# Kernel tuning notes

Hardware: AMD Instinct MI355X
Metric: run time of the kernel (lower is better)

## Reference

```python
import jax, jax.numpy as jnp
import numpy as np

ANCHOR_SIZES = (128.0, 256.0, 512.0)
ASPECT_RATIOS = (0.5, 1.0, 2.0)
NMS_THR = 0.7
KEEP_PRE = 1000    # test_keep_pre_nms
KEEP_POST = 300    # test_keep_post_nms


def make_anchors(fh, fw, img_h, img_w):
    # base anchors per (ratio, size), centered at origin, xyxy
    sizes = jnp.array(ANCHOR_SIZES, jnp.float32)
    ratios = jnp.array(ASPECT_RATIOS, jnp.float32)
    h_r = jnp.sqrt(ratios)
    w_r = 1.0 / h_r
    ws = (w_r[:, None] * sizes[None, :]).reshape(-1)  # [nA]
    hs = (h_r[:, None] * sizes[None, :]).reshape(-1)
    base = jnp.stack([-ws, -hs, ws, hs], axis=1) / 2.0  # [nA,4]
    stride_h = img_h / fh
    stride_w = img_w / fw
    sx = jnp.arange(fw, dtype=jnp.float32) * stride_w
    sy = jnp.arange(fh, dtype=jnp.float32) * stride_h
    yy, xx = jnp.meshgrid(sy, sx, indexing='ij')
    shifts = jnp.stack([xx, yy, xx, yy], axis=-1).reshape(-1, 1, 4)  # [fh*fw,1,4]
    return (shifts + base[None]).reshape(-1, 4)  # [fh*fw*nA,4]


def offsets2boxes(deltas, anchors):
    # deltas: [bs,N,4] (dx,dy,dw,dh); anchors: [N,4] xyxy
    aw = anchors[:, 2] - anchors[:, 0]
    ah = anchors[:, 3] - anchors[:, 1]
    acx = anchors[:, 0] + 0.5 * aw
    acy = anchors[:, 1] + 0.5 * ah
    pcx = deltas[..., 0] * aw + acx
    pcy = deltas[..., 1] * ah + acy
    pw = jnp.exp(deltas[..., 2]) * aw
    ph = jnp.exp(deltas[..., 3]) * ah
    return jnp.stack([pcx - 0.5 * pw, pcy - 0.5 * ph,
                      pcx + 0.5 * pw, pcy + 0.5 * ph], axis=-1)


def nms_single(boxes, scores):
    # boxes [K,4] already sorted by descending score; sequential greedy NMS
    K = boxes.shape[0]
    b = jax.lax.stop_gradient(boxes)
    area = (b[:, 2] - b[:, 0]) * (b[:, 3] - b[:, 1])
    lt = jnp.maximum(b[:, None, :2], b[None, :, :2])
    rb = jnp.minimum(b[:, None, 2:], b[None, :, 2:])
    wh = jnp.clip(rb - lt, 0.0)
    inter = wh[..., 0] * wh[..., 1]
    iou = inter / (area[:, None] + area[None, :] - inter + 1e-9)  # [K,K]
    idx = jnp.arange(K)

    def body(i, keep):
        suppress = (iou[i] > NMS_THR) & keep[i] & (idx > i)
        return keep & ~suppress

    keep = jax.lax.fori_loop(0, K, body, jnp.ones((K,), bool))
    # stable: kept boxes first, preserving score order; pad to KEEP_POST
    order = jnp.argsort((~keep).astype(jnp.int32))[:KEEP_POST]
    valid = keep[order].astype(boxes.dtype)
    dets = jnp.concatenate([boxes[order], scores[order, None]], axis=-1)
    return dets * valid[:, None]  # padded rows are zeros


def setup_inputs() -> dict:
    key = jax.random.key(0)
    ks = jax.random.split(key, 4)
    C = 512
    nA = 9
    return {
        'fmaps': jax.random.normal(ks[0], (8, C, 64, 64), jnp.float32),
        'base_w': jax.random.normal(ks[1], (C, C, 3, 3), jnp.float32) * 0.01,
        'base_b': jnp.zeros((C,), jnp.float32),
        'cls_w': jax.random.normal(ks[2], (nA, C), jnp.float32) * 0.01,
        'cls_b': jnp.zeros((nA,), jnp.float32),
        'reg_w': jax.random.normal(ks[3], (nA * 4, C), jnp.float32) * 0.01,
        'reg_b': jnp.zeros((nA * 4,), jnp.float32),
        'img_h': 1024,
        'img_w': 1024,
    }


def reference(fmaps, base_w, base_b, cls_w, cls_b, reg_w, reg_b, img_h, img_w):
    bs, C, fh, fw = fmaps.shape
    nA = len(ANCHOR_SIZES) * len(ASPECT_RATIOS)
    # PredictionLayer: 3x3 conv + relu, then 1x1 cls / reg convs
    x = jax.lax.conv_general_dilated(
        fmaps, base_w, window_strides=(1, 1), padding='SAME',
        dimension_numbers=('NCHW', 'OIHW', 'NCHW'))
    x = jax.nn.relu(x + base_b[None, :, None, None])
    cls = jnp.einsum('bchw,ac->bahw', x, cls_w) + cls_b[None, :, None, None]
    reg = jnp.einsum('bchw,ac->bahw', x, reg_w) + reg_b[None, :, None, None]
    # flatten_preds: view(bs,nA,c,h,w) -> permute(0,3,4,1,2) -> (bs, h*w*nA, c)
    cls_logits = cls.reshape(bs, nA, 1, fh, fw).transpose(0, 3, 4, 1, 2).reshape(bs, -1, 1)
    reg_deltas = reg.reshape(bs, nA, 4, fh, fw).transpose(0, 3, 4, 1, 2).reshape(bs, -1, 4)
    # DetectionLayer
    anchors = make_anchors(fh, fw, float(img_h), float(img_w))
    scores = jax.nn.sigmoid(cls_logits[..., 0])          # [bs, N]
    boxes = offsets2boxes(reg_deltas, anchors)           # [bs, N, 4]
    _, sel = jax.lax.top_k(scores, KEEP_PRE)             # per-image top-k
    s = jnp.take_along_axis(scores, sel, axis=1)
    b = jnp.take_along_axis(boxes, sel[..., None], axis=1)
    # clip boxes to image
    b = jnp.stack([jnp.clip(b[..., 0], 0.0, float(img_w)),
                   jnp.clip(b[..., 1], 0.0, float(img_h)),
                   jnp.clip(b[..., 2], 0.0, float(img_w)),
                   jnp.clip(b[..., 3], 0.0, float(img_h))], axis=-1)
    # per-image NMS; output padded to fixed [bs, KEEP_POST, 5]
    return jax.vmap(nms_single)(b, s)
```

## Files before the change

kernel.cpp:

```cpp
#include <hip/hip_runtime.h>
#include <math.h>


typedef double f64x4 __attribute__((ext_vector_type(4)));
typedef double f64x2 __attribute__((ext_vector_type(2)));

#define BS 8
#define CIN 512
#define COUT 512
#define FH 64
#define FW 64
#define NA 9
#define NPIX (FH*FW)
#define NANCH (NPIX*NA)
#define NPAD 65536
#define KPRE 1000
#define KPOST 300

#define OFF_X      0ull
#define OFF_SCORES (OFF_X + 134217728ull)
#define OFF_BOXES  (OFF_SCORES + 2359296ull)
#define OFF_KEYS   (OFF_BOXES + 9437184ull)
#define OFF_BUF1   (OFF_KEYS + 4194304ull)
#define OFF_BUF2   (OFF_BUF1 + 1048576ull)
#define OFF_SEL    (OFF_BUF2 + 262144ull)
#define OFF_KEEP   (OFF_SEL + 32768ull)
#define WS_NEEDED  (OFF_KEEP + 32768ull)
#define OFF_MASK   OFF_X
#define WOFF_U        WS_NEEDED
#define WOFF_V        (WOFF_U + 33554432ull)
#define WS_WINO_FULL  (WOFF_V + 67108864ull + 67108864ull)
#define WS_WINO_HALF  (WOFF_V + 33554432ull + 33554432ull)

#define SW_STRIDE 80
#define SW_WORDS  (36 * SW_STRIDE)
#define SI_RSTRIDE 80
#define SI_CSTRIDE 320
#define BUF_WORDS (SW_WORDS + 4 * SI_CSTRIDE)

__device__ __forceinline__ void conv_compute(
    const float* __restrict__ sWp, const float* __restrict__ sIp,
    const int* __restrict__ boff, f64x4 acc[2][4]) {
#pragma unroll
  for (int k0s = 0; k0s < 9; ++k0s) {
    double a0 = (double)sWp[k0s * 4 * SW_STRIDE];
    double a1 = (double)sWp[k0s * 4 * SW_STRIDE + 16];
    const float* bp = sIp + boff[k0s];
    double b0 = (double)bp[0];
    double b1 = (double)bp[16];
    double b2 = (double)bp[32];
    double b3 = (double)bp[48];
    acc[0][0] = __builtin_amdgcn_mfma_f64_16x16x4f64(a0, b0, acc[0][0], 0, 0, 0);
    acc[0][1] = __builtin_amdgcn_mfma_f64_16x16x4f64(a0, b1, acc[0][1], 0, 0, 0);
    acc[0][2] = __builtin_amdgcn_mfma_f64_16x16x4f64(a0, b2, acc[0][2], 0, 0, 0);
    acc[0][3] = __builtin_amdgcn_mfma_f64_16x16x4f64(a0, b3, acc[0][3], 0, 0, 0);
    acc[1][0] = __builtin_amdgcn_mfma_f64_16x16x4f64(a1, b0, acc[1][0], 0, 0, 0);
    acc[1][1] = __builtin_amdgcn_mfma_f64_16x16x4f64(a1, b1, acc[1][1], 0, 0, 0);
    acc[1][2] = __builtin_amdgcn_mfma_f64_16x16x4f64(a1, b2, acc[1][2], 0, 0, 0);
    acc[1][3] = __builtin_amdgcn_mfma_f64_16x16x4f64(a1, b3, acc[1][3], 0, 0, 0);
  }
}

__global__ __launch_bounds__(256, 3) void conv_mfma_kernel(
    const float* __restrict__ fm, const float* __restrict__ W,
    const float* __restrict__ bias, double* __restrict__ x) {
  __shared__ float sbuf[2 * BUF_WORDS];
  const int ocb = blockIdx.x, rp = blockIdx.y, b = blockIdx.z;
  const int h0 = rp * 2;
  const int oc0 = ocb * 64;
  const int tid = threadIdx.x;
  const int wid = tid >> 6, l = tid & 63;
  const int q = l >> 4, r16 = l & 15;
  const int wm = wid >> 1, wn = wid & 1;

  const int wo = tid >> 2, wseg = tid & 3;
  const float* wbase = W + (size_t)(oc0 + wo) * 4608 + wseg * 9;
  const int wlds0 = (wseg * 9) * SW_STRIDE + wo;

  const float* fmb = fm + (size_t)b * CIN * NPIX;
  int ioff[5];
  int idls[5];
  bool sact[5], lact[5];
#pragma unroll
  for (int s = 0; s < 5; ++s) {
    int li = tid + 256 * s;
    sact[s] = li < 1056;
    int li_c = sact[s] ? li : 0;
    int c = li_c / 264, rem = li_c % 264, r = rem / 66, col = rem % 66;
    int gy = h0 - 1 + r, gx = col - 1;
    lact[s] = sact[s] && gy >= 0 && gy < FH && gx >= 0 && gx < FW;
    ioff[s] = lact[s] ? (c * NPIX + gy * FW + gx) : 0;
    idls[s] = SW_WORDS + c * SI_CSTRIDE + r * SI_RSTRIDE + col;
  }

  const int apos = q * SW_STRIDE + wm * 32 + r16;
  const int ipos = SW_WORDS + wn * SI_RSTRIDE + r16;
  int boff[9];
#pragma unroll
  for (int k0s = 0; k0s < 9; ++k0s) {
    int k = k0s * 4 + q;
    int c = k / 9, t = k - 9 * c;
    int dy = t / 3, dx = t - 3 * dy;
    boff[k0s] = c * SI_CSTRIDE + dy * SI_RSTRIDE + dx;
  }

  f64x4 acc[2][4];
#pragma unroll
  for (int tm = 0; tm < 2; ++tm)
#pragma unroll
    for (int tn = 0; tn < 4; ++tn)
#pragma unroll
      for (int v = 0; v < 4; ++v) acc[tm][tn][v] = 0.0;

  float wreg[9], ireg[5];

#define LOAD_REGS(t) do {                                            \
    const int cc_ = 4 * (t);                                         \
    _Pragma("unroll")                                                \
    for (int j = 0; j < 9; ++j) wreg[j] = wbase[cc_ * 9 + j];        \
    _Pragma("unroll")                                                \
    for (int s = 0; s < 5; ++s)                                      \
      ireg[s] = lact[s] ? fmb[(size_t)(ioff[s] + cc_ * NPIX)] : 0.f; \
  } while (0)

#define WRITE_LDS(base) do {                                         \
    _Pragma("unroll")                                                \
    for (int j = 0; j < 9; ++j) (base)[wlds0 + j * SW_STRIDE] = wreg[j]; \
    _Pragma("unroll")                                                \
    for (int s = 0; s < 5; ++s)                                      \
      if (sact[s]) (base)[idls[s]] = ireg[s];                        \
  } while (0)

  float* buf0 = sbuf;
  float* buf1 = sbuf + BUF_WORDS;

  LOAD_REGS(0);
  WRITE_LDS(buf0);
  __syncthreads();

  for (int tt = 0; tt < 64; ++tt) {
    const int t1 = 2 * tt + 1;
    LOAD_REGS(t1);
    __builtin_amdgcn_s_setprio(1);
    conv_compute(buf0 + apos, buf0 + ipos, boff, acc);
    __builtin_amdgcn_s_setprio(0);
    WRITE_LDS(buf1);
    __syncthreads();
    const int t2 = (t1 + 1 < 128) ? t1 + 1 : 127;
    LOAD_REGS(t2);
    __builtin_amdgcn_s_setprio(1);
    conv_compute(buf1 + apos, buf1 + ipos, boff, acc);
    __builtin_amdgcn_s_setprio(0);
    WRITE_LDS(buf0);
    __syncthreads();
  }

  int prow[4], pcol[4];
  {
    f64x4 probe = {0.0, 0.0, 0.0, 0.0};
    double pa = (q == 0) ? (double)r16 : ((q == 1) ? 1.0 : 0.0);
    double pb = (q == 0) ? 1.0 : ((q == 1) ? (double)(16 * r16) : 0.0);
    probe = __builtin_amdgcn_mfma_f64_16x16x4f64(pa, pb, probe, 0, 0, 0);
#pragma unroll
    for (int v = 0; v < 4; ++v) {
      int val = (int)(probe[v] + 0.5);
      prow[v] = val & 15;
      pcol[v] = (val >> 4) & 15;
    }
  }

#pragma unroll
  for (int tm = 0; tm < 2; ++tm) {
#pragma unroll
    for (int v = 0; v < 4; ++v) {
      const int oc = oc0 + wm * 32 + tm * 16 + prow[v];
      const double bv = (double)bias[oc];
      const int h = h0 + wn;
#pragma unroll
      for (int tn = 0; tn < 4; ++tn) {
        const int w = tn * 16 + pcol[v];
        double val = acc[tm][tn][v] + bv;
        val = val > 0.0 ? val : 0.0;
        x[(size_t)(b * COUT + oc) * NPIX + h * FW + w] = val;
      }
    }
  }
#undef LOAD_REGS
#undef WRITE_LDS
}

__global__ __launch_bounds__(256) void wino_wt_kernel(
    const float* __restrict__ W, double* __restrict__ U) {
  const int id = blockIdx.x * 256 + threadIdx.x;
  const int oc = id >> 9, c = id & 511;
  const float* g = W + (size_t)(oc * CIN + c) * 9;
  double g0[3], g1[3], g2[3];
#pragma unroll
  for (int j = 0; j < 3; ++j) {
    g0[j] = (double)g[j];
    g1[j] = (double)g[3 + j];
    g2[j] = (double)g[6 + j];
  }
  double T[4][3];
#pragma unroll
  for (int j = 0; j < 3; ++j) {
    T[0][j] = g0[j];
    T[1][j] = 0.5 * (g0[j] + g1[j] + g2[j]);
    T[2][j] = 0.5 * (g0[j] - g1[j] + g2[j]);
    T[3][j] = g2[j];
  }
  double* Ub = U + (size_t)c * 512 + oc;
#pragma unroll
  for (int xi = 0; xi < 4; ++xi) {
    double u0 = T[xi][0];
    double u1 = 0.5 * (T[xi][0] + T[xi][1] + T[xi][2]);
    double u2 = 0.5 * (T[xi][0] - T[xi][1] + T[xi][2]);
    double u3 = T[xi][2];
    Ub[(size_t)(xi * 4 + 0) * 262144] = u0;
    Ub[(size_t)(xi * 4 + 1) * 262144] = u1;
    Ub[(size_t)(xi * 4 + 2) * 262144] = u2;
    Ub[(size_t)(xi * 4 + 3) * 262144] = u3;
  }
}

template <int T>
__global__ __launch_bounds__(256) void wino_in_kernel(
    const float* __restrict__ fm, double* __restrict__ V, int b, int t0) {
  const int id = blockIdx.x * 256 + threadIdx.x;
  const int c = id / T, rem = id % T;
  const int tyx = t0 + rem;
  const int ty = tyx >> 5, tx = tyx & 31;
  const float* src = fm + (size_t)(b * CIN + c) * NPIX;
  const int y0 = 2 * ty - 1, x0 = 2 * tx - 1;
  double d[4][4];
#pragma unroll
  for (int r = 0; r < 4; ++r) {
    int y = y0 + r;
#pragma unroll
    for (int s = 0; s < 4; ++s) {
      int xx = x0 + s;
      d[r][s] = (y >= 0 && y < FH && xx >= 0 && xx < FW)
                    ? (double)src[y * FW + xx] : 0.0;
    }
  }
  double Z[4][4];
#pragma unroll
  for (int s = 0; s < 4; ++s) {
    Z[0][s] = d[0][s] - d[2][s];
    Z[1][s] = d[1][s] + d[2][s];
    Z[2][s] = d[2][s] - d[1][s];
    Z[3][s] = d[1][s] - d[3][s];
  }
  double* Vb = V + (size_t)c * T + rem;
#pragma unroll
  for (int xi = 0; xi < 4; ++xi) {
    double v0 = Z[xi][0] - Z[xi][2];
    double v1 = Z[xi][1] + Z[xi][2];
    double v2 = Z[xi][2] - Z[xi][1];
    double v3 = Z[xi][1] - Z[xi][3];
    Vb[(size_t)(xi * 4 + 0) * 512 * T] = v0;
    Vb[(size_t)(xi * 4 + 1) * 512 * T] = v1;
    Vb[(size_t)(xi * 4 + 2) * 512 * T] = v2;
    Vb[(size_t)(xi * 4 + 3) * 512 * T] = v3;
  }
}

#define WSU_STRIDE 72
#define WSV_STRIDE 136
#define WSU_WORDS  (8 * WSU_STRIDE)
#define WBUF_WORDS (WSU_WORDS + 8 * WSV_STRIDE)

__device__ __forceinline__ void wino_compute(
    const double* __restrict__ sA, const double* __restrict__ sB,
    f64x4 acc[2][4]) {
#pragma unroll
  for (int kg = 0; kg < 2; ++kg) {
    double a0 = sA[kg * 4 * WSU_STRIDE];
    double a1 = sA[kg * 4 * WSU_STRIDE + 16];
    const double* bp = sB + kg * 4 * WSV_STRIDE;
    double b0 = bp[0];
    double b1 = bp[16];
    double b2 = bp[32];
    double b3 = bp[48];
    acc[0][0] = __builtin_amdgcn_mfma_f64_16x16x4f64(a0, b0, acc[0][0], 0, 0, 0);
    acc[0][1] = __builtin_amdgcn_mfma_f64_16x16x4f64(a0, b1, acc[0][1], 0, 0, 0);
    acc[0][2] = __builtin_amdgcn_mfma_f64_16x16x4f64(a0, b2, acc[0][2], 0, 0, 0);
    acc[0][3] = __builtin_amdgcn_mfma_f64_16x16x4f64(a0, b3, acc[0][3], 0, 0, 0);
    acc[1][0] = __builtin_amdgcn_mfma_f64_16x16x4f64(a1, b0, acc[1][0], 0, 0, 0);
    acc[1][1] = __builtin_amdgcn_mfma_f64_16x16x4f64(a1, b1, acc[1][1], 0, 0, 0);
    acc[1][2] = __builtin_amdgcn_mfma_f64_16x16x4f64(a1, b2, acc[1][2], 0, 0, 0);
    acc[1][3] = __builtin_amdgcn_mfma_f64_16x16x4f64(a1, b3, acc[1][3], 0, 0, 0);
  }
}

template <int T>
__global__ __launch_bounds__(256, 3) void wino_gemm_kernel(
    const double* __restrict__ U, const double* __restrict__ V,
    double* __restrict__ M) {
  __shared__ double sbuf[2 * WBUF_WORDS];
  const int ocb = blockIdx.x, tb = blockIdx.y, pos = blockIdx.z;
  const int oc0 = ocb * 64, t0 = tb * 128;
  const int tid = threadIdx.x;
  const int wid = tid >> 6, l = tid & 63;
  const int q = l >> 4, r16 = l & 15;
  const int wm = wid >> 1, wn = wid & 1;

  const int ka = tid >> 5;
  const int oc2 = (tid & 31) * 2;
  const int t4 = (tid & 31) * 4;
  const double* uSrc = U + (size_t)pos * 262144 + (size_t)ka * 512 + oc0 + oc2;
  const double* vSrc = V + (size_t)pos * 512 * T + (size_t)ka * T + t0 + t4;
  const int ua_lds = ka * WSU_STRIDE + oc2;
  const int vb_lds = WSU_WORDS + ka * WSV_STRIDE + t4;

  const int apos = q * WSU_STRIDE + wm * 32 + r16;
  const int bpos = WSU_WORDS + q * WSV_STRIDE + wn * 64 + r16;

  f64x4 acc[2][4];
#pragma unroll
  for (int tm = 0; tm < 2; ++tm)
#pragma unroll
    for (int tn = 0; tn < 4; ++tn)
#pragma unroll
      for (int v = 0; v < 4; ++v) acc[tm][tn][v] = 0.0;

  f64x2 ra, rb0, rb1;

#define WLOAD(t) do {                                                  \
    const size_t cc_ = 8 * (size_t)(t);                                \
    ra  = *(const f64x2*)(uSrc + cc_ * 512);                           \
    rb0 = *(const f64x2*)(vSrc + cc_ * T);                             \
    rb1 = *(const f64x2*)(vSrc + cc_ * T + 2);                         \
  } while (0)

#define WSTORE(base) do {                                              \
    (base)[ua_lds] = ra[0]; (base)[ua_lds + 1] = ra[1];                \
    (base)[vb_lds] = rb0[0]; (base)[vb_lds + 1] = rb0[1];              \
    (base)[vb_lds + 2] = rb1[0]; (base)[vb_lds + 3] = rb1[1];          \
  } while (0)

  double* buf0 = sbuf;
  double* buf1 = sbuf + WBUF_WORDS;

  WLOAD(0);
  WSTORE(buf0);
  __syncthreads();

  for (int tt = 0; tt < 32; ++tt) {
    const int t1 = 2 * tt + 1;
    WLOAD(t1);
    __builtin_amdgcn_s_setprio(1);
    wino_compute(buf0 + apos, buf0 + bpos, acc);
    __builtin_amdgcn_s_setprio(0);
    WSTORE(buf1);
    __syncthreads();
    const int t2 = (t1 + 1 < 64) ? t1 + 1 : 63;
    WLOAD(t2);
    __builtin_amdgcn_s_setprio(1);
    wino_compute(buf1 + apos, buf1 + bpos, acc);
    __builtin_amdgcn_s_setprio(0);
    WSTORE(buf0);
    __syncthreads();
  }

  int prow[4], pcol[4];
  {
    f64x4 probe = {0.0, 0.0, 0.0, 0.0};
    double pa = (q == 0) ? (double)r16 : ((q == 1) ? 1.0 : 0.0);
    double pb = (q == 0) ? 1.0 : ((q == 1) ? (double)(16 * r16) : 0.0);
    probe = __builtin_amdgcn_mfma_f64_16x16x4f64(pa, pb, probe, 0, 0, 0);
#pragma unroll
    for (int v = 0; v < 4; ++v) {
      int val = (int)(probe[v] + 0.5);
      prow[v] = val & 15;
      pcol[v] = (val >> 4) & 15;
    }
  }

#pragma unroll
  for (int tm = 0; tm < 2; ++tm) {
#pragma unroll
    for (int v = 0; v < 4; ++v) {
      const int oc = oc0 + wm * 32 + tm * 16 + prow[v];
#pragma unroll
      for (int tn = 0; tn < 4; ++tn) {
        const int col = wn * 64 + tn * 16 + pcol[v];
        M[(size_t)pos * 512 * T + (size_t)oc * T + t0 + col] = acc[tm][tn][v];
      }
    }
  }
#undef WLOAD
#undef WSTORE
}

template <int T>
__global__ __launch_bounds__(256) void wino_out_kernel(
    const double* __restrict__ M, const float* __restrict__ bias,
    double* __restrict__ x, int b, int t0) {
  const int id = blockIdx.x * 256 + threadIdx.x;
  const int oc = id / T, rem = id % T;
  const int tyx = t0 + rem;
  const int ty = tyx >> 5, tx = tyx & 31;
  double m[4][4];
#pragma unroll
  for (int xi = 0; xi < 4; ++xi)
#pragma unroll
    for (int nu = 0; nu < 4; ++nu)
      m[xi][nu] = M[(size_t)(xi * 4 + nu) * 512 * T + (size_t)oc * T + rem];
  double P[2][4];
#pragma unroll
  for (int nu = 0; nu < 4; ++nu) {
    P[0][nu] = m[0][nu] + m[1][nu] + m[2][nu];
    P[1][nu] = m[1][nu] - m[2][nu] - m[3][nu];
  }
  const double bv = (double)bias[oc];
  double* xb = x + (size_t)(b * COUT + oc) * NPIX + (2 * ty) * FW + 2 * tx;
#pragma unroll
  for (int i = 0; i < 2; ++i) {
    double y0 = P[i][0] + P[i][1] + P[i][2] + bv;
    double y1 = P[i][1] - P[i][2] - P[i][3] + bv;
    y0 = y0 > 0.0 ? y0 : 0.0;
    y1 = y1 > 0.0 ? y1 : 0.0;
    xb[i * FW] = y0;
    xb[i * FW + 1] = y1;
  }
}

__global__ __launch_bounds__(256) void heads_kernel(
    const double* __restrict__ x, const float* __restrict__ cls_w,
    const float* __restrict__ cls_b, const float* __restrict__ reg_w,
    const float* __restrict__ reg_b, const int* __restrict__ img_h,
    const int* __restrict__ img_w, double* __restrict__ scores,
    double* __restrict__ boxes, unsigned long long* __restrict__ keys) {
  __shared__ double sx[4096];
  __shared__ double swl[2880];
  const int b = blockIdx.x >> 6;
  const int ptile = blockIdx.x & 63;
  const int tx = threadIdx.x, ty = threadIdx.y;
  const int tid = ty * 64 + tx;

  double acc[12];
#pragma unroll
  for (int j = 0; j < 12; ++j) acc[j] = 0.0;

  for (int cc = 0; cc < CIN; cc += 64) {
    for (int li = tid; li < 4096; li += 256) {
      int ci = li >> 6, px = li & 63;
      sx[li] = x[((long)b * CIN + cc + ci) * NPIX + ptile * 64 + px];
    }
    for (int li = tid; li < 2880; li += 256) {
      int o = li >> 6, ci = li & 63;
      float wv = (o < 9) ? cls_w[o * CIN + cc + ci] : reg_w[(o - 9) * CIN + cc + ci];
      swl[li] = (double)wv;
    }
    __syncthreads();
#pragma unroll 4
    for (int ci = 0; ci < 64; ++ci) {
      double xv = sx[ci * 64 + tx];
#pragma unroll
      for (int j = 0; j < 12; ++j) {
        int o = ty + 4 * j;
        if (o < 45) acc[j] += swl[o * 64 + ci] * xv;
      }
    }
    __syncthreads();
  }

#pragma unroll
  for (int j = 0; j < 12; ++j) {
    int o = ty + 4 * j;
    if (o < 45) {
      double bv = (o < 9) ? (double)cls_b[o] : (double)reg_b[o - 9];
      swl[o * 64 + tx] = acc[j] + bv;
    }
  }
  __syncthreads();

  const double ih = (double)img_h[0], iw = (double)img_w[0];
  const double sth = ih / (double)FH, stw = iw / (double)FW;
  const double ratios[3] = {0.5, 1.0, 2.0};
  const double sizes[3] = {128.0, 256.0, 512.0};

  for (int it = tid; it < 576; it += 256) {
    int px = it / 9, a = it % 9;
    int p = ptile * 64 + px;
    int hh = p >> 6, ww = p & 63;
    double z = swl[a * 64 + px];
    double score = 1.0 / (1.0 + exp(-z));
    double d0 = swl[(9 + a * 4 + 0) * 64 + px];
    double d1 = swl[(9 + a * 4 + 1) * 64 + px];
    double d2 = swl[(9 + a * 4 + 2) * 64 + px];
    double d3 = swl[(9 + a * 4 + 3) * 64 + px];
    double ratio = ratios[a / 3], size = sizes[a % 3];
    double hr = sqrt(ratio), wr = 1.0 / hr;
    double wsz = wr * size, hsz = hr * size;
    double sxc = (double)ww * stw, syc = (double)hh * sth;
    double ax0 = sxc - wsz * 0.5, ax1 = sxc + wsz * 0.5;
    double ay0 = syc - hsz * 0.5, ay1 = syc + hsz * 0.5;
    double aw = ax1 - ax0, ah = ay1 - ay0;
    double acx = ax0 + 0.5 * aw, acy = ay0 + 0.5 * ah;
    double pcx = d0 * aw + acx, pcy = d1 * ah + acy;
    double pw = exp(d2) * aw, ph = exp(d3) * ah;
    double bx0 = pcx - 0.5 * pw, by0 = pcy - 0.5 * ph;
    double bx1 = pcx + 0.5 * pw, by1 = pcy + 0.5 * ph;
    bx0 = fmin(fmax(bx0, 0.0), iw); bx1 = fmin(fmax(bx1, 0.0), iw);
    by0 = fmin(fmax(by0, 0.0), ih); by1 = fmin(fmax(by1, 0.0), ih);
    long n = (long)p * 9 + a;
    long base = (long)b * NANCH + n;
    boxes[base * 4 + 0] = bx0; boxes[base * 4 + 1] = by0;
    boxes[base * 4 + 2] = bx1; boxes[base * 4 + 3] = by1;
    scores[base] = score;
    unsigned long long bits = (unsigned long long)__double_as_longlong(score);
    keys[(long)b * NPAD + n] =
        ~((bits & 0xFFFFFFFFFFFF0000ull) | (0xFFFFull - (unsigned long long)n));
  }
}

__device__ inline void bitonic4096(unsigned long long* s, int tid) {
  for (int k = 2; k <= 4096; k <<= 1) {
    for (int j = k >> 1; j > 0; j >>= 1) {
#pragma unroll 2
      for (int t = tid; t < 2048; t += 1024) {
        int i = ((t & ~(j - 1)) << 1) | (t & (j - 1));
        int p = i | j;
        bool up = ((i & k) == 0);
        unsigned long long a = s[i], c = s[p];
        if ((a > c) == up) { s[i] = c; s[p] = a; }
      }
      __syncthreads();
    }
  }
}

__global__ __launch_bounds__(1024) void sort_topk_kernel(
    const unsigned long long* __restrict__ in, unsigned long long* __restrict__ out,
    long in_stride, long out_stride) {
  __shared__ unsigned long long s[4096];
  const int b = blockIdx.y, q = blockIdx.x, tid = threadIdx.x;
  const unsigned long long* ip = in + (long)b * in_stride + (long)q * 4096;
#pragma unroll 4
  for (int l = tid; l < 4096; l += 1024) s[l] = ip[l];
  __syncthreads();
  bitonic4096(s, tid);
  unsigned long long* op = out + (long)b * out_stride + (long)q * 1024;
  op[tid] = s[tid];
}

__global__ __launch_bounds__(1024) void sort_final_kernel(
    const unsigned long long* __restrict__ in, int* __restrict__ sel) {
  __shared__ unsigned long long s[4096];
  const int b = blockIdx.x, tid = threadIdx.x;
  const unsigned long long* ip = in + (long)b * 4096;
#pragma unroll 4
  for (int l = tid; l < 4096; l += 1024) s[l] = ip[l];
  __syncthreads();
  bitonic4096(s, tid);
  if (tid < KPRE) sel[b * 1024 + tid] = (int)(s[tid] & 0xFFFFull);
}

__global__ __launch_bounds__(256) void nms_mask_kernel(
    const double* __restrict__ boxes, const int* __restrict__ sel,
    unsigned long long* __restrict__ mask) {
  __shared__ double X0[KPRE], Y0[KPRE], X1[KPRE], Y1[KPRE], AR[KPRE];
  const int ig = blockIdx.x, b = blockIdx.y, tid = threadIdx.x;
  for (int r = tid; r < KPRE; r += 256) {
    int n = sel[b * 1024 + r];
    const double* bp = boxes + ((long)b * NANCH + n) * 4;
    double x0 = bp[0], y0 = bp[1], x1 = bp[2], y1 = bp[3];
    X0[r] = x0; Y0[r] = y0; X1[r] = x1; Y1[r] = y1;
    AR[r] = (x1 - x0) * (y1 - y0);
  }
  __syncthreads();
  const int i = ig * 16 + (tid >> 4);
  const int w = tid & 15;
  if (i >= KPRE) return;
  const double xi0 = X0[i], yi0 = Y0[i], xi1 = X1[i], yi1 = Y1[i], ai = AR[i];
  unsigned long long m = 0;
#pragma unroll 8
  for (int jj = 0; jj < 64; ++jj) {
    int jo = (jj + w) & 63;
    int j = w * 64 + jo;
    if (j < KPRE && j > i) {
      double lx = fmax(xi0, X0[j]), ly = fmax(yi0, Y0[j]);
      double rx = fmin(xi1, X1[j]), ry = fmin(yi1, Y1[j]);
      double ww_ = fmax(rx - lx, 0.0);
      double hh_ = fmax(ry - ly, 0.0);
      double inter = ww_ * hh_;
      double iou = inter / (ai + AR[j] - inter + 1e-9);
      if (iou > 0.7) m |= (1ull << jo);
    }
  }
  mask[((size_t)b * 1024 + i) * 16 + w] = m;
}

__global__ __launch_bounds__(256) void nms_scan_kernel(
    const unsigned long long* __restrict__ mask, int* __restrict__ keep) {
  __shared__ unsigned long long smask[KPRE * 16];
  __shared__ unsigned long long skeep[16];
  const int b = blockIdx.x, tid = threadIdx.x;
  const unsigned long long* mb = mask + (size_t)b * 1024 * 16;
  for (int l = tid; l < KPRE * 16; l += 256) smask[l] = mb[(l / 16) * 16 + (l & 15)];
  if (tid < 16) skeep[tid] = ~0ull;
  __syncthreads();
  if (tid < 64) {
    for (int i = 0; i < KPRE; ++i) {
      unsigned long long kw = skeep[i >> 6];
      if ((kw >> (i & 63)) & 1ull) {
        if (tid < 16) skeep[tid] &= ~smask[i * 16 + tid];
      }
    }
  }
  __syncthreads();
  for (int r = tid; r < KPRE; r += 256)
    keep[b * 1024 + r] = (int)((skeep[r >> 6] >> (r & 63)) & 1ull);
}

__global__ __launch_bounds__(1024) void out_kernel(
    const double* __restrict__ boxes, const double* __restrict__ scores,
    const int* __restrict__ sel, const int* __restrict__ keep,
    float* __restrict__ out) {
  const int b = blockIdx.x, tid = threadIdx.x;
  int kv = (tid < KPRE) ? keep[b * 1024 + tid] : 0;
  unsigned long long m = __ballot(kv != 0);
  int lane = tid & 63, wid = tid >> 6;
  __shared__ int wcnt[16], woff[16], tot;
  if (lane == 0) wcnt[wid] = __popcll(m);
  __syncthreads();
  if (tid == 0) {
    int s = 0;
    for (int w2 = 0; w2 < 16; ++w2) { woff[w2] = s; s += wcnt[w2]; }
    tot = s;
  }
  __syncthreads();
  int before = __popcll(m & ((1ull << lane) - 1ull));
  int pref = woff[wid] + before;
  if (tid < KPRE) {
    int pos = kv ? pref : (tot + (tid - pref));
    if (pos < KPOST) {
      float* o = out + ((long)b * KPOST + pos) * 5;
      if (kv) {
        int n = sel[b * 1024 + tid];
        const double* bp = boxes + ((long)b * NANCH + n) * 4;
        o[0] = (float)bp[0]; o[1] = (float)bp[1];
        o[2] = (float)bp[2]; o[3] = (float)bp[3];
        o[4] = (float)scores[(long)b * NANCH + n];
      } else {
        o[0] = 0.f; o[1] = 0.f; o[2] = 0.f; o[3] = 0.f; o[4] = 0.f;
      }
    }
  }
}

extern "C" void kernel_launch(void* const* d_in, const int* in_sizes, int n_in,
                              void* d_out, int out_size, void* d_ws, size_t ws_size,
                              hipStream_t stream) {
  const float* fm     = (const float*)d_in[0];
  const float* base_w = (const float*)d_in[1];
  const float* base_b = (const float*)d_in[2];
  const float* cls_w  = (const float*)d_in[3];
  const float* cls_b  = (const float*)d_in[4];
  const float* reg_w  = (const float*)d_in[5];
  const float* reg_b  = (const float*)d_in[6];
  const int* img_h    = (const int*)d_in[7];
  const int* img_w    = (const int*)d_in[8];
  float* out          = (float*)d_out;

  if (ws_size < WS_NEEDED) return;

  char* ws = (char*)d_ws;
  double* x                 = (double*)(ws + OFF_X);
  double* scores            = (double*)(ws + OFF_SCORES);
  double* boxes             = (double*)(ws + OFF_BOXES);
  unsigned long long* keys  = (unsigned long long*)(ws + OFF_KEYS);
  unsigned long long* buf1  = (unsigned long long*)(ws + OFF_BUF1);
  unsigned long long* buf2  = (unsigned long long*)(ws + OFF_BUF2);
  int* sel                  = (int*)(ws + OFF_SEL);
  int* keep                 = (int*)(ws + OFF_KEEP);
  unsigned long long* mask  = (unsigned long long*)(ws + OFF_MASK);

  hipMemsetAsync(ws + OFF_KEYS, 0xFF, 4194304ull + 1048576ull, stream);

  if (ws_size >= WS_WINO_FULL) {
    double* U = (double*)(ws + WOFF_U);
    double* V = (double*)(ws + WOFF_V);
    double* M = (double*)(ws + WOFF_V + 67108864ull);
    wino_wt_kernel<<<dim3(1024), dim3(256), 0, stream>>>(base_w, U);
    for (int b = 0; b < BS; ++b) {
      wino_in_kernel<1024><<<dim3(2048), dim3(256), 0, stream>>>(fm, V, b, 0);
      wino_gemm_kernel<1024><<<dim3(8, 8, 16), dim3(256), 0, stream>>>(U, V, M);
      wino_out_kernel<1024><<<dim3(2048), dim3(256), 0, stream>>>(M, base_b, x, b, 0);
    }
  } else if (ws_size >= WS_WINO_HALF) {
    double* U = (double*)(ws + WOFF_U);
    double* V = (double*)(ws + WOFF_V);
    double* M = (double*)(ws + WOFF_V + 33554432ull);
    wino_wt_kernel<<<dim3(1024), dim3(256), 0, stream>>>(base_w, U);
    for (int b = 0; b < BS; ++b) {
      for (int t0 = 0; t0 < 1024; t0 += 512) {
        wino_in_kernel<512><<<dim3(1024), dim3(256), 0, stream>>>(fm, V, b, t0);
        wino_gemm_kernel<512><<<dim3(8, 4, 16), dim3(256), 0, stream>>>(U, V, M);
        wino_out_kernel<512><<<dim3(1024), dim3(256), 0, stream>>>(M, base_b, x, b, t0);
      }
    }
  } else {
    conv_mfma_kernel<<<dim3(8, 32, 8), dim3(256), 0, stream>>>(fm, base_w, base_b, x);
  }

  heads_kernel<<<dim3(512), dim3(64, 4), 0, stream>>>(
      x, cls_w, cls_b, reg_w, reg_b, img_h, img_w, scores, boxes, keys);
  sort_topk_kernel<<<dim3(9, 8), dim3(1024), 0, stream>>>(keys, buf1, 65536, 16384);
  sort_topk_kernel<<<dim3(4, 8), dim3(1024), 0, stream>>>(buf1, buf2, 16384, 4096);
  sort_final_kernel<<<dim3(8), dim3(1024), 0, stream>>>(buf2, sel);
  nms_mask_kernel<<<dim3(64, 8), dim3(256), 0, stream>>>(boxes, sel, mask);
  nms_scan_kernel<<<dim3(8), dim3(256), 0, stream>>>(mask, keep);
  out_kernel<<<dim3(8), dim3(1024), 0, stream>>>(boxes, scores, sel, keep, out);
}
```

Baseline: 1.986 ms.

## Rewrite RPN heads 1x1 conv as double-buffered FP64 MFMA GEMM

Replaces the scalar FMA loop in the heads kernel with FP64 16x16x4 MFMA instructions over 16-channel K slices. The x and weight tiles are staged through double-buffered padded LDS, with register prefetch of the next slice overlapping compute. An MFMA probe recovers the accumulator row/column layout for the epilogue write to LDS. This targets the compute-bound 45-output head GEMM, at the cost of padding outputs to 48 and making more sync rounds (32 K slices instead of 8).

```diff
diff --git a/kernel.cpp b/kernel.cpp
--- a/kernel.cpp
+++ b/kernel.cpp
@@ -426,52 +426,133 @@
   }
 }
 
-__global__ __launch_bounds__(256) void heads_kernel(
+#define HX_STRIDE 72
+#define HW_STRIDE 52
+#define HSX_WORDS (16 * HX_STRIDE)
+#define HBUF_WORDS (HSX_WORDS + 16 * HW_STRIDE)
+
+__device__ __forceinline__ void heads_compute(
+    const double* __restrict__ sA, const double* __restrict__ sB,
+    f64x4 acc[3]) {
+#pragma unroll
+  for (int k0s = 0; k0s < 4; ++k0s) {
+    double a0 = sA[k0s * 4 * HW_STRIDE];
+    double a1 = sA[k0s * 4 * HW_STRIDE + 16];
+    double a2 = sA[k0s * 4 * HW_STRIDE + 32];
+    double b0 = sB[k0s * 4 * HX_STRIDE];
+    acc[0] = __builtin_amdgcn_mfma_f64_16x16x4f64(a0, b0, acc[0], 0, 0, 0);
+    acc[1] = __builtin_amdgcn_mfma_f64_16x16x4f64(a1, b0, acc[1], 0, 0, 0);
+    acc[2] = __builtin_amdgcn_mfma_f64_16x16x4f64(a2, b0, acc[2], 0, 0, 0);
+  }
+}
+
+__global__ __launch_bounds__(256) void heads_mfma_kernel(
     const double* __restrict__ x, const float* __restrict__ cls_w,
     const float* __restrict__ cls_b, const float* __restrict__ reg_w,
     const float* __restrict__ reg_b, const int* __restrict__ img_h,
     const int* __restrict__ img_w, double* __restrict__ scores,
     double* __restrict__ boxes, unsigned long long* __restrict__ keys) {
-  __shared__ double sx[4096];
-  __shared__ double swl[2880];
-  const int b = blockIdx.x >> 6;
-  const int ptile = blockIdx.x & 63;
-  const int tx = threadIdx.x, ty = threadIdx.y;
-  const int tid = ty * 64 + tx;
-
-  double acc[12];
-#pragma unroll
-  for (int j = 0; j < 12; ++j) acc[j] = 0.0;
-
-  for (int cc = 0; cc < CIN; cc += 64) {
-    for (int li = tid; li < 4096; li += 256) {
-      int ci = li >> 6, px = li & 63;
-      sx[li] = x[((long)b * CIN + cc + ci) * NPIX + ptile * 64 + px];
-    }
-    for (int li = tid; li < 2880; li += 256) {
-      int o = li >> 6, ci = li & 63;
-      float wv = (o < 9) ? cls_w[o * CIN + cc + ci] : reg_w[(o - 9) * CIN + cc + ci];
-      swl[li] = (double)wv;
-    }
+  __shared__ double sh[2 * HBUF_WORDS];
+  const int pxb = blockIdx.x, b = blockIdx.y;
+  const int tid = threadIdx.x;
+  const int wid = tid >> 6, l = tid & 63;
+  const int q = l >> 4, r16 = l & 15;
+  const int wn = wid;
+
+  const double* xbase = x + (size_t)b * CIN * NPIX + pxb * 64;
+  int sxk[4], sxp[4];
+#pragma unroll
+  for (int s = 0; s < 4; ++s) {
+    int i = tid + 256 * s;
+    sxk[s] = i >> 6; sxp[s] = i & 63;
+  }
+  int swk[3], swo[3];
+#pragma unroll
+  for (int s = 0; s < 3; ++s) {
+    int i = tid + 256 * s;
+    swk[s] = i / 48; swo[s] = i % 48;
+  }
+
+  const int aposh = HSX_WORDS + q * HW_STRIDE + r16;
+  const int bposh = q * HX_STRIDE + wn * 16 + r16;
+
+  f64x4 acc[3];
+#pragma unroll
+  for (int mt = 0; mt < 3; ++mt)
+#pragma unroll
+    for (int v = 0; v < 4; ++v) acc[mt][v] = 0.0;
+
+  double xr[4], wr[3];
+
+#define HLOAD(t) do {                                                    \
+    const int cc_ = 16 * (t);                                            \
+    _Pragma("unroll")                                                    \
+    for (int s = 0; s < 4; ++s)                                          \
+      xr[s] = xbase[(size_t)(cc_ + sxk[s]) * NPIX + sxp[s]];             \
+    _Pragma("unroll")                                                    \
+    for (int s = 0; s < 3; ++s) {                                        \
+      int o = swo[s], k = cc_ + swk[s];                                  \
+      wr[s] = (o < 9) ? (double)cls_w[o * CIN + k]                       \
+            : (o < 45) ? (double)reg_w[(o - 9) * CIN + k] : 0.0;         \
+    }                                                                    \
+  } while (0)
+
+#define HSTORE(base) do {                                                \
+    _Pragma("unroll")                                                    \
+    for (int s = 0; s < 4; ++s) (base)[sxk[s] * HX_STRIDE + sxp[s]] = xr[s]; \
+    _Pragma("unroll")                                                    \
+    for (int s = 0; s < 3; ++s)                                          \
+      (base)[HSX_WORDS + swk[s] * HW_STRIDE + swo[s]] = wr[s];           \
+  } while (0)
+
+  double* buf0 = sh;
+  double* buf1 = sh + HBUF_WORDS;
+
+  HLOAD(0);
+  HSTORE(buf0);
+  __syncthreads();
+
+  for (int tt = 0; tt < 16; ++tt) {
+    const int t1 = 2 * tt + 1;
+    HLOAD(t1);
+    __builtin_amdgcn_s_setprio(1);
+    heads_compute(buf0 + aposh, buf0 + bposh, acc);
+    __builtin_amdgcn_s_setprio(0);
+    HSTORE(buf1);
     __syncthreads();
-#pragma unroll 4
-    for (int ci = 0; ci < 64; ++ci) {
-      double xv = sx[ci * 64 + tx];
-#pragma unroll
-      for (int j = 0; j < 12; ++j) {
-        int o = ty + 4 * j;
-        if (o < 45) acc[j] += swl[o * 64 + ci] * xv;
+    const int t2 = (t1 + 1 < 32) ? t1 + 1 : 31;
+    HLOAD(t2);
+    __builtin_amdgcn_s_setprio(1);
+    heads_compute(buf1 + aposh, buf1 + bposh, acc);
+    __builtin_amdgcn_s_setprio(0);
+    HSTORE(buf0);
+    __syncthreads();
+  }
+
+  int prow[4], pcol[4];
+  {
+    f64x4 probe = {0.0, 0.0, 0.0, 0.0};
+    double pa = (q == 0) ? (double)r16 : ((q == 1) ? 1.0 : 0.0);
+    double pb = (q == 0) ? 1.0 : ((q == 1) ? (double)(16 * r16) : 0.0);
+    probe = __builtin_amdgcn_mfma_f64_16x16x4f64(pa, pb, probe, 0, 0, 0);
+#pragma unroll
+    for (int v = 0; v < 4; ++v) {
+      int val = (int)(probe[v] + 0.5);
+      prow[v] = val & 15;
+      pcol[v] = (val >> 4) & 15;
+    }
+  }
+
+  double* slog = sh;
+#pragma unroll
+  for (int mt = 0; mt < 3; ++mt) {
+#pragma unroll
+    for (int v = 0; v < 4; ++v) {
+      const int o = mt * 16 + prow[v];
+      if (o < 45) {
+        double bv = (o < 9) ? (double)cls_b[o] : (double)reg_b[o - 9];
+        slog[o * HX_STRIDE + wn * 16 + pcol[v]] = acc[mt][v] + bv;
       }
-    }
-    __syncthreads();
-  }
-
-#pragma unroll
-  for (int j = 0; j < 12; ++j) {
-    int o = ty + 4 * j;
-    if (o < 45) {
-      double bv = (o < 9) ? (double)cls_b[o] : (double)reg_b[o - 9];
-      swl[o * 64 + tx] = acc[j] + bv;
     }
   }
   __syncthreads();
@@ -483,17 +564,17 @@
 
   for (int it = tid; it < 576; it += 256) {
     int px = it / 9, a = it % 9;
-    int p = ptile * 64 + px;
+    int p = pxb * 64 + px;
     int hh = p >> 6, ww = p & 63;
-    double z = swl[a * 64 + px];
+    double z = slog[a * HX_STRIDE + px];
     double score = 1.0 / (1.0 + exp(-z));
-    double d0 = swl[(9 + a * 4 + 0) * 64 + px];
-    double d1 = swl[(9 + a * 4 + 1) * 64 + px];
-    double d2 = swl[(9 + a * 4 + 2) * 64 + px];
-    double d3 = swl[(9 + a * 4 + 3) * 64 + px];
+    double d0 = slog[(9 + a * 4 + 0) * HX_STRIDE + px];
+    double d1 = slog[(9 + a * 4 + 1) * HX_STRIDE + px];
+    double d2 = slog[(9 + a * 4 + 2) * HX_STRIDE + px];
+    double d3 = slog[(9 + a * 4 + 3) * HX_STRIDE + px];
     double ratio = ratios[a / 3], size = sizes[a % 3];
-    double hr = sqrt(ratio), wr = 1.0 / hr;
-    double wsz = wr * size, hsz = hr * size;
+    double hr = sqrt(ratio), wr_ = 1.0 / hr;
+    double wsz = wr_ * size, hsz = hr * size;
     double sxc = (double)ww * stw, syc = (double)hh * sth;
     double ax0 = sxc - wsz * 0.5, ax1 = sxc + wsz * 0.5;
     double ay0 = syc - hsz * 0.5, ay1 = syc + hsz * 0.5;
@@ -514,6 +595,8 @@
     keys[(long)b * NPAD + n] =
         ~((bits & 0xFFFFFFFFFFFF0000ull) | (0xFFFFull - (unsigned long long)n));
   }
+#undef HLOAD
+#undef HSTORE
 }
 
 __device__ inline void bitonic4096(unsigned long long* s, int tid) {
@@ -706,7 +789,7 @@
     conv_mfma_kernel<<<dim3(8, 32, 8), dim3(256), 0, stream>>>(fm, base_w, base_b, x);
   }
 
-  heads_kernel<<<dim3(512), dim3(64, 4), 0, stream>>>(
+  heads_mfma_kernel<<<dim3(64, 8), dim3(256), 0, stream>>>(
       x, cls_w, cls_b, reg_w, reg_b, img_h, img_w, scores, boxes, keys);
   sort_topk_kernel<<<dim3(9, 8), dim3(1024), 0, stream>>>(keys, buf1, 65536, 16384);
   sort_topk_kernel<<<dim3(4, 8), dim3(1024), 0, stream>>>(buf1, buf2, 16384, 4096);
```

New measurement: 1.777 ms. 10.5% less time.
